# Kernel optimization log

Measured on AMD Instinct MI355X. Metric: run time of the kernel, lower is better.

Reference implementation:

```python
import jax, jax.numpy as jnp
import numpy as np

B, S, D, H = 2, 2048, 1024, 16
HD = D // H  # head dim = 64


def setup_inputs() -> dict:
    key = jax.random.key(0)
    ks = jax.random.split(key, 8)
    s = 0.02
    return {
        "Q": jax.random.normal(ks[0], (B, S, D), jnp.float32),
        "K": jax.random.normal(ks[1], (B, S, D), jnp.float32),
        "V": jax.random.normal(ks[2], (B, S, D), jnp.float32),
        "mask": jax.random.randint(ks[3], (1, 1, S, S), 0, 2, jnp.int32),
        "Wq": jax.random.normal(ks[4], (D, D), jnp.float32) * s,
        "bq": jnp.zeros((D,), jnp.float32),
        "Wk": jax.random.normal(ks[5], (D, D), jnp.float32) * s,
        "bk": jnp.zeros((D,), jnp.float32),
        "Wv": jax.random.normal(ks[6], (D, D), jnp.float32) * s,
        "bv": jnp.zeros((D,), jnp.float32),
        "Wo": jax.random.normal(ks[7], (D, D), jnp.float32) * s,
        "bo": jnp.zeros((D,), jnp.float32),
    }


def reference(Q, K, V, mask, Wq, bq, Wk, bk, Wv, bv, Wo, bo):
    b = Q.shape[0]
    # QKV projections, split into heads: [B,S,D] -> [B,H,S,HD]
    q = (Q @ Wq + bq).reshape(b, -1, H, HD).transpose(0, 2, 1, 3)
    k = (K @ Wk + bk).reshape(b, -1, H, HD).transpose(0, 2, 1, 3)
    v = (V @ Wv + bv).reshape(b, -1, H, HD).transpose(0, 2, 1, 3)
    # scaled dot-product attention with full [B,H,S,S] scores (as in source)
    scale = jnp.sqrt(jnp.asarray(HD, q.dtype))
    scores = jnp.einsum("bhqd,bhkd->bhqk", q, k) / scale
    scores = jnp.where(mask == 0, -jnp.inf, scores)
    attn = jax.nn.softmax(scores, axis=-1)
    ctx = jnp.einsum("bhqk,bhkd->bhqd", attn, v)
    # merge heads and output projection
    concat = ctx.transpose(0, 2, 1, 3).reshape(b, -1, H * HD)
    return concat @ Wo + bo
```

## Files before the change

kernel.cpp:

```cpp
#include <hip/hip_runtime.h>


using s8v = __attribute__((ext_vector_type(8))) short;
using f4v = __attribute__((ext_vector_type(4))) float;
typedef unsigned long long u64;

__device__ __forceinline__ unsigned short f2bf(float f) {
  union { float f; unsigned int u; } v; v.f = f;
  return (unsigned short)((v.u + 0x7fffu + ((v.u >> 16) & 1u)) >> 16);
}

__device__ __forceinline__ void gll16(const void* g, void* l) {
  __builtin_amdgcn_global_load_lds(
      (const __attribute__((address_space(1))) unsigned int*)g,
      (__attribute__((address_space(3))) unsigned int*)l, 16, 0, 0);
}

__global__ void prep_kernel(const float* __restrict__ Q, const float* __restrict__ K,
                            const float* __restrict__ V,
                            unsigned short* __restrict__ qb, unsigned short* __restrict__ kb,
                            unsigned short* __restrict__ vb,
                            const float* __restrict__ W0, const float* __restrict__ W1,
                            const float* __restrict__ W2, const float* __restrict__ W3,
                            unsigned short* __restrict__ T0, unsigned short* __restrict__ T1,
                            unsigned short* __restrict__ T2, unsigned short* __restrict__ T3,
                            const int* __restrict__ mask, u64* __restrict__ bm) {
  __shared__ unsigned short t[64][72];
  const int bid = blockIdx.x, tid = threadIdx.x;
  if (bid < 12288) {
    int z = bid >> 12;
    int idx = (bid & 4095) * 256 + tid;
    const float* in = (z == 0) ? Q : (z == 1) ? K : V;
    unsigned short* out = (z == 0) ? qb : (z == 1) ? kb : vb;
    float4 v = ((const float4*)in)[idx];
    ushort4 o;
    o.x = f2bf(v.x); o.y = f2bf(v.y); o.z = f2bf(v.z); o.w = f2bf(v.w);
    ((ushort4*)out)[idx] = o;
  } else if (bid < 13312) {
    int b = bid - 12288;
    int z = b >> 8, rem = b & 255;
    int k0 = (rem >> 4) * 64, n0 = (rem & 15) * 64;
    const float* W = (z == 0) ? W0 : (z == 1) ? W1 : (z == 2) ? W2 : W3;
    unsigned short* Wt = (z == 0) ? T0 : (z == 1) ? T1 : (z == 2) ? T2 : T3;
    for (int p = 0; p < 4; ++p) {
      int idx = p * 256 + tid;
      int row = idx >> 4, c4 = idx & 15;
      float4 v = *(const float4*)&W[(size_t)(k0 + row) * 1024 + n0 + c4 * 4];
      t[row][c4 * 4 + 0] = f2bf(v.x);
      t[row][c4 * 4 + 1] = f2bf(v.y);
      t[row][c4 * 4 + 2] = f2bf(v.z);
      t[row][c4 * 4 + 3] = f2bf(v.w);
    }
    __syncthreads();
    for (int p = 0; p < 2; ++p) {
      int idx = p * 256 + tid;
      int j = idx >> 3, c8 = idx & 7;
      unsigned short tmp[8];
      for (int i = 0; i < 8; ++i) tmp[i] = t[c8 * 8 + i][j];
      uint4 o;
      o.x = tmp[0] | ((unsigned)tmp[1] << 16);
      o.y = tmp[2] | ((unsigned)tmp[3] << 16);
      o.z = tmp[4] | ((unsigned)tmp[5] << 16);
      o.w = tmp[6] | ((unsigned)tmp[7] << 16);
      *(uint4*)&Wt[(size_t)(n0 + j) * 1024 + k0 + c8 * 8] = o;
    }
  } else {
    int b = bid - 13312;
    int gw = (b * 256 + tid) >> 6;
    int lane = tid & 63;
    int mv = mask[(size_t)gw * 64 + lane];
    u64 bal = __ballot(mv != 0);
    if (lane == 0) bm[gw] = bal;
  }
}

__global__ __launch_bounds__(256) void proj3_kernel(
    const unsigned short* __restrict__ A0, const unsigned short* __restrict__ A1,
    const unsigned short* __restrict__ A2,
    const unsigned short* __restrict__ W0, const unsigned short* __restrict__ W1,
    const unsigned short* __restrict__ W2,
    const float* __restrict__ b0, const float* __restrict__ b1, const float* __restrict__ b2,
    unsigned short* __restrict__ oq, unsigned short* __restrict__ ok,
    unsigned short* __restrict__ ovt) {
  const int z = blockIdx.z;
  const unsigned short* A  = (z == 0) ? A0 : (z == 1) ? A1 : A2;
  const unsigned short* Wt = (z == 0) ? W0 : (z == 1) ? W1 : W2;
  const float* bias        = (z == 0) ? b0 : (z == 1) ? b1 : b2;

  __shared__ __align__(16) unsigned short As[64 * 32];
  __shared__ __align__(16) unsigned short Bs[128 * 32];

  const int tid = threadIdx.x;
  const int lane = tid & 63, w = tid >> 6, ln = lane & 15, quad = lane >> 4;
  const int wm = (w & 1) * 32, wn = (w >> 1) * 64;
  const int m0 = blockIdx.x * 64, n0 = blockIdx.y * 128;

  const int slr = lane >> 2;
  const int schunk = (lane & 3) ^ ((lane >> 3) & 3);
  const int cfrag = (quad ^ ((ln >> 1) & 3)) * 8;

  f4v zero = {0.f, 0.f, 0.f, 0.f};
  f4v acc[2][4];
  for (int mi = 0; mi < 2; ++mi)
    for (int ni = 0; ni < 4; ++ni) acc[mi][ni] = zero;

  for (int kt = 0; kt < 1024; kt += 32) {
    __syncthreads();
    gll16(&A[(size_t)(m0 + w * 16 + slr) * 1024 + kt + schunk * 8],        &As[(w * 16) * 32]);
    gll16(&Wt[(size_t)(n0 + w * 32 + slr) * 1024 + kt + schunk * 8],       &Bs[(w * 32) * 32]);
    gll16(&Wt[(size_t)(n0 + w * 32 + 16 + slr) * 1024 + kt + schunk * 8],  &Bs[(w * 32 + 16) * 32]);
    __syncthreads();
    s8v a[2], b[4];
    for (int mi = 0; mi < 2; ++mi) a[mi] = *(const s8v*)&As[(wm + mi * 16 + ln) * 32 + cfrag];
    for (int ni = 0; ni < 4; ++ni) b[ni] = *(const s8v*)&Bs[(wn + ni * 16 + ln) * 32 + cfrag];
    if (z < 2) {
      for (int mi = 0; mi < 2; ++mi)
        for (int ni = 0; ni < 4; ++ni)
          acc[mi][ni] = __builtin_amdgcn_mfma_f32_16x16x32_bf16(a[mi], b[ni], acc[mi][ni], 0, 0, 0);
    } else {
      for (int mi = 0; mi < 2; ++mi)
        for (int ni = 0; ni < 4; ++ni)
          acc[mi][ni] = __builtin_amdgcn_mfma_f32_16x16x32_bf16(b[ni], a[mi], acc[mi][ni], 0, 0, 0);
    }
  }

  if (z < 2) {
    const float qscale = (z == 0) ? 0.18033688f : 1.0f;
    unsigned short* outp = (z == 0) ? oq : ok;
    for (int mi = 0; mi < 2; ++mi) {
      int rb = m0 + wm + mi * 16 + quad * 4;
      int b_ = rb >> 11;
      for (int ni = 0; ni < 4; ++ni) {
        int col = n0 + wn + ni * 16 + ln;
        float bvv = bias[col];
        int h = col >> 6, hd = col & 63;
        size_t ob = (size_t)(b_ * 16 + h) * 2048;
        for (int r = 0; r < 4; ++r) {
          int s = (rb + r) & 2047;
          outp[(ob + s) * 64 + hd] = f2bf((acc[mi][ni][r] + bvv) * qscale);
        }
      }
    }
  } else {
    for (int ni = 0; ni < 4; ++ni) {
      for (int r = 0; r < 4; ++r) {
        int colw = n0 + wn + ni * 16 + quad * 4 + r;
        int h = colw >> 6, hd = colw & 63;
        float bvv = bias[colw];
        for (int mi = 0; mi < 2; ++mi) {
          int sg = m0 + wm + mi * 16 + ln;
          int b_ = sg >> 11, ss = sg & 2047;
          ovt[((size_t)(b_ * 16 + h) * 64 + hd) * 2048 + ss] = f2bf(acc[mi][ni][r] + bvv);
        }
      }
    }
  }
}

__global__ __launch_bounds__(256) void flash_kernel(
    const unsigned short* __restrict__ q, const unsigned short* __restrict__ k,
    const unsigned short* __restrict__ vt, const u64* __restrict__ bm,
    unsigned short* __restrict__ ctx) {
  __shared__ __align__(16) unsigned short qp_s[128][72];
  __shared__ __align__(16) unsigned short k_s[64][72];
  __shared__ __align__(16) unsigned short v_s[80][72];

  const int tid = threadIdx.x;
  const int lane = tid & 63, w = tid >> 6, ln = lane & 15, quad = lane >> 4;
  const int q0 = blockIdx.x * 128;
  const int bh = blockIdx.y;
  const unsigned short* qg  = q  + ((size_t)bh * 2048 + q0) * 64;
  const unsigned short* kgb = k  + (size_t)bh * 2048 * 64;
  const unsigned short* vgb = vt + (size_t)bh * 64 * 2048;

  for (int j = 0; j < 5; ++j) {
    int idx = j * 256 + tid;
    if (idx < 16 * 72) ((unsigned short*)v_s[64])[idx] = 0;
  }
  for (int p = 0; p < 4; ++p) {
    int c = p * 256 + tid;
    int row = c >> 3, c8 = c & 7;
    *(uint4*)&qp_s[row][c8 * 8] = *(const uint4*)&qg[(size_t)row * 64 + c8 * 8];
  }
  __syncthreads();
  if (tid < 64) v_s[64][tid] = 0x3F80;
  __syncthreads();

  s8v aq[2][2];
  for (int s = 0; s < 2; ++s)
    for (int h = 0; h < 2; ++h)
      aq[s][h] = *(const s8v*)&qp_s[s * 64 + w * 16 + ln][h * 32 + quad * 8];
  s8v bones0 = *(const s8v*)&v_s[64 + ln][quad * 8];
  s8v bones1 = *(const s8v*)&v_s[64 + ln][32 + quad * 8];

  const int srow0 = tid >> 3, sc8 = tid & 7;
  const int srow1 = 32 + srow0;

  const u64* bmr0 = bm + (size_t)(q0 + w * 16 + ln) * 32;
  const u64* bmr1 = bmr0 + 64 * 32;

  uint4 kr0 = *(const uint4*)&kgb[(size_t)srow0 * 64 + sc8 * 8];
  uint4 kr1 = *(const uint4*)&kgb[(size_t)srow1 * 64 + sc8 * 8];
  uint4 vr0 = *(const uint4*)&vgb[(size_t)srow0 * 2048 + sc8 * 8];
  uint4 vr1 = *(const uint4*)&vgb[(size_t)srow1 * 2048 + sc8 * 8];
  u64 mwc[2], mwn[2];
  mwc[0] = bmr0[0];
  mwc[1] = bmr1[0];

  f4v zero = {0.f, 0.f, 0.f, 0.f};
  f4v l_acc[2];
  f4v o_acc[2][4];
  for (int s = 0; s < 2; ++s) {
    l_acc[s] = zero;
    for (int ni = 0; ni < 4; ++ni) o_acc[s][ni] = zero;
  }

  for (int kt = 0; kt < 2048; kt += 64) {
    *(uint4*)&k_s[srow0][sc8 * 8] = kr0;
    *(uint4*)&k_s[srow1][sc8 * 8] = kr1;
    *(uint4*)&v_s[srow0][sc8 * 8] = vr0;
    *(uint4*)&v_s[srow1][sc8 * 8] = vr1;
    if (kt + 64 < 2048) {
      int ktn = kt + 64;
      kr0 = *(const uint4*)&kgb[(size_t)(ktn + srow0) * 64 + sc8 * 8];
      kr1 = *(const uint4*)&kgb[(size_t)(ktn + srow1) * 64 + sc8 * 8];
      vr0 = *(const uint4*)&vgb[(size_t)srow0 * 2048 + ktn + sc8 * 8];
      vr1 = *(const uint4*)&vgb[(size_t)srow1 * 2048 + ktn + sc8 * 8];
      int ktcn = ktn >> 6;
      mwn[0] = bmr0[ktcn];
      mwn[1] = bmr1[ktcn];
    }
    __syncthreads();

    f4v sc[2][4];
    for (int ni = 0; ni < 4; ++ni) {
      s8v ak0 = *(const s8v*)&k_s[ni * 16 + ln][quad * 8];
      s8v ak1 = *(const s8v*)&k_s[ni * 16 + ln][32 + quad * 8];
      for (int s = 0; s < 2; ++s) {
        f4v t = zero;
        t = __builtin_amdgcn_mfma_f32_16x16x32_bf16(ak0, aq[s][0], t, 0, 0, 0);
        t = __builtin_amdgcn_mfma_f32_16x16x32_bf16(ak1, aq[s][1], t, 0, 0, 0);
        sc[s][ni] = t;
      }
    }

    for (int s = 0; s < 2; ++s) {
      u64 m = mwc[s] >> (quad * 4);
      unsigned mlo = (unsigned)m, mhi = (unsigned)(m >> 32);
      for (int ni = 0; ni < 4; ++ni) {
        unsigned msel = ((ni < 2) ? mlo : mhi) >> ((ni & 1) * 16);
        unsigned u0 = __float_as_uint(__builtin_amdgcn_exp2f(sc[s][ni][0]) * (float)(msel & 1u));
        unsigned u1 = __float_as_uint(__builtin_amdgcn_exp2f(sc[s][ni][1]) * (float)((msel >> 1) & 1u));
        unsigned u2 = __float_as_uint(__builtin_amdgcn_exp2f(sc[s][ni][2]) * (float)((msel >> 2) & 1u));
        unsigned u3 = __float_as_uint(__builtin_amdgcn_exp2f(sc[s][ni][3]) * (float)((msel >> 3) & 1u));
        unsigned plo = __builtin_amdgcn_perm(u1, u0, 0x07060302);
        unsigned phi = __builtin_amdgcn_perm(u3, u2, 0x07060302);
        *(u64*)&qp_s[s * 64 + w * 16 + ln][ni * 16 + quad * 4] = plo | ((u64)phi << 32);
      }
      mwc[s] = mwn[s];
    }

    s8v ap[2][2];
    for (int s = 0; s < 2; ++s)
      for (int h = 0; h < 2; ++h)
        ap[s][h] = *(const s8v*)&qp_s[s * 64 + w * 16 + ln][h * 32 + quad * 8];
    for (int ni = 0; ni < 4; ++ni) {
      s8v bv0 = *(const s8v*)&v_s[ni * 16 + ln][quad * 8];
      s8v bv1 = *(const s8v*)&v_s[ni * 16 + ln][32 + quad * 8];
      for (int s = 0; s < 2; ++s) {
        o_acc[s][ni] = __builtin_amdgcn_mfma_f32_16x16x32_bf16(ap[s][0], bv0, o_acc[s][ni], 0, 0, 0);
        o_acc[s][ni] = __builtin_amdgcn_mfma_f32_16x16x32_bf16(ap[s][1], bv1, o_acc[s][ni], 0, 0, 0);
      }
    }
    for (int s = 0; s < 2; ++s) {
      l_acc[s] = __builtin_amdgcn_mfma_f32_16x16x32_bf16(ap[s][0], bones0, l_acc[s], 0, 0, 0);
      l_acc[s] = __builtin_amdgcn_mfma_f32_16x16x32_bf16(ap[s][1], bones1, l_acc[s], 0, 0, 0);
    }
    __syncthreads();
  }

  int b_ = bh >> 4, h = bh & 15;
  for (int s = 0; s < 2; ++s) {
    for (int r = 0; r < 4; ++r) {
      float lr = __shfl(l_acc[s][r], quad * 16);
      float inv = 1.f / lr;
      int srow = q0 + s * 64 + w * 16 + quad * 4 + r;
      size_t base = ((size_t)b_ * 2048 + srow) * 1024 + h * 64;
      for (int ni = 0; ni < 4; ++ni)
        ctx[base + ni * 16 + ln] = f2bf(o_acc[s][ni][r] * inv);
    }
  }
}

__global__ __launch_bounds__(256) void gemm_out_kernel(
    const unsigned short* __restrict__ A, const unsigned short* __restrict__ Wt,
    const float* __restrict__ bias, float* __restrict__ out) {
  __shared__ __align__(16) unsigned short As[64 * 32];
  __shared__ __align__(16) unsigned short Bs[128 * 32];

  const int tid = threadIdx.x;
  const int lane = tid & 63, w = tid >> 6, ln = lane & 15, quad = lane >> 4;
  const int wm = (w & 1) * 32, wn = (w >> 1) * 64;
  const int m0 = blockIdx.x * 64, n0 = blockIdx.y * 128;

  const int slr = lane >> 2;
  const int schunk = (lane & 3) ^ ((lane >> 3) & 3);
  const int cfrag = (quad ^ ((ln >> 1) & 3)) * 8;

  f4v zero = {0.f, 0.f, 0.f, 0.f};
  f4v acc[2][4];
  for (int mi = 0; mi < 2; ++mi)
    for (int ni = 0; ni < 4; ++ni) acc[mi][ni] = zero;

  for (int kt = 0; kt < 1024; kt += 32) {
    __syncthreads();
    gll16(&A[(size_t)(m0 + w * 16 + slr) * 1024 + kt + schunk * 8],        &As[(w * 16) * 32]);
    gll16(&Wt[(size_t)(n0 + w * 32 + slr) * 1024 + kt + schunk * 8],       &Bs[(w * 32) * 32]);
    gll16(&Wt[(size_t)(n0 + w * 32 + 16 + slr) * 1024 + kt + schunk * 8],  &Bs[(w * 32 + 16) * 32]);
    __syncthreads();
    s8v a[2], b[4];
    for (int mi = 0; mi < 2; ++mi) a[mi] = *(const s8v*)&As[(wm + mi * 16 + ln) * 32 + cfrag];
    for (int ni = 0; ni < 4; ++ni) b[ni] = *(const s8v*)&Bs[(wn + ni * 16 + ln) * 32 + cfrag];
    for (int mi = 0; mi < 2; ++mi)
      for (int ni = 0; ni < 4; ++ni)
        acc[mi][ni] = __builtin_amdgcn_mfma_f32_16x16x32_bf16(a[mi], b[ni], acc[mi][ni], 0, 0, 0);
  }

  for (int mi = 0; mi < 2; ++mi) {
    int rb = m0 + wm + mi * 16 + quad * 4;
    for (int ni = 0; ni < 4; ++ni) {
      int col = n0 + wn + ni * 16 + ln;
      float bvv = bias[col];
      for (int r = 0; r < 4; ++r)
        out[(size_t)(rb + r) * 1024 + col] = acc[mi][ni][r] + bvv;
    }
  }
}

extern "C" void kernel_launch(void* const* d_in, const int* in_sizes, int n_in,
                              void* d_out, int out_size, void* d_ws, size_t ws_size,
                              hipStream_t stream) {
  const float* Q  = (const float*)d_in[0];
  const float* K  = (const float*)d_in[1];
  const float* V  = (const float*)d_in[2];
  const int* mask = (const int*)d_in[3];
  const float* Wq = (const float*)d_in[4];
  const float* bq = (const float*)d_in[5];
  const float* Wk = (const float*)d_in[6];
  const float* bk = (const float*)d_in[7];
  const float* Wv = (const float*)d_in[8];
  const float* bv = (const float*)d_in[9];
  const float* Wo = (const float*)d_in[10];
  const float* bo = (const float*)d_in[11];
  float* out = (float*)d_out;

  char* ws = (char*)d_ws;
  const size_t MB = 1u << 20;
  unsigned short* qb  = (unsigned short*)(ws + 0 * MB);
  unsigned short* kb  = (unsigned short*)(ws + 8 * MB);
  unsigned short* vb  = (unsigned short*)(ws + 16 * MB);
  unsigned short* wqt = (unsigned short*)(ws + 24 * MB);
  unsigned short* wkt = (unsigned short*)(ws + 26 * MB);
  unsigned short* wvt = (unsigned short*)(ws + 28 * MB);
  unsigned short* wot = (unsigned short*)(ws + 30 * MB);
  unsigned short* qh  = (unsigned short*)(ws + 32 * MB);
  unsigned short* kh  = (unsigned short*)(ws + 40 * MB);
  unsigned short* vth = (unsigned short*)(ws + 48 * MB);
  u64* bm             = (u64*)(ws + 56 * MB);
  unsigned short* ctx = (unsigned short*)(ws + 16 * MB);

  prep_kernel<<<29696, 256, 0, stream>>>(Q, K, V, qb, kb, vb,
                                         Wq, Wk, Wv, Wo, wqt, wkt, wvt, wot,
                                         mask, bm);
  proj3_kernel<<<dim3(64, 8, 3), 256, 0, stream>>>(qb, kb, vb, wqt, wkt, wvt,
                                                   bq, bk, bv, qh, kh, vth);
  flash_kernel<<<dim3(16, 32), 256, 0, stream>>>(qh, kh, vth, bm, ctx);
  gemm_out_kernel<<<dim3(64, 8), 256, 0, stream>>>(ctx, wot, bo, out);
}
```

Before: 260.8 us.

## Split attention over key halves with atomic accumulation and add combine kernel

The flash kernel now splits the key dimension into two chunks, doubling the grid to 1024 blocks. Each block atomically adds its unnormalized output and row-sum into fp32 global buffers. A new combine kernel normalizes these and writes the bf16 context. This is valid without a running max only because the code never subtracts one, so partial sums add directly. It also swaps grid x/y ordering in the projection and output GEMMs so blocks sharing the same M-tile run adjacently. The aim is better CU occupancy on the attention stage, at the cost of two memsets, atomic traffic and an extra kernel launch.

```diff
diff --git a/kernel.cpp b/kernel.cpp
--- a/kernel.cpp
+++ b/kernel.cpp
@@ -93,7 +93,7 @@
   const int tid = threadIdx.x;
   const int lane = tid & 63, w = tid >> 6, ln = lane & 15, quad = lane >> 4;
   const int wm = (w & 1) * 32, wn = (w >> 1) * 64;
-  const int m0 = blockIdx.x * 64, n0 = blockIdx.y * 128;
+  const int n0 = blockIdx.x * 128, m0 = blockIdx.y * 64;
 
   const int slr = lane >> 2;
   const int schunk = (lane & 3) ^ ((lane >> 3) & 3);
@@ -160,18 +160,19 @@
 __global__ __launch_bounds__(256) void flash_kernel(
     const unsigned short* __restrict__ q, const unsigned short* __restrict__ k,
     const unsigned short* __restrict__ vt, const u64* __restrict__ bm,
-    unsigned short* __restrict__ ctx) {
+    float* __restrict__ o_glob, float* __restrict__ l_glob) {
   __shared__ __align__(16) unsigned short qp_s[128][72];
   __shared__ __align__(16) unsigned short k_s[64][72];
   __shared__ __align__(16) unsigned short v_s[80][72];
 
   const int tid = threadIdx.x;
   const int lane = tid & 63, w = tid >> 6, ln = lane & 15, quad = lane >> 4;
-  const int q0 = blockIdx.x * 128;
+  const int qt = blockIdx.x & 15, kc = blockIdx.x >> 4;
+  const int q0 = qt * 128;
   const int bh = blockIdx.y;
   const unsigned short* qg  = q  + ((size_t)bh * 2048 + q0) * 64;
-  const unsigned short* kgb = k  + (size_t)bh * 2048 * 64;
-  const unsigned short* vgb = vt + (size_t)bh * 64 * 2048;
+  const unsigned short* kgb = k  + ((size_t)bh * 2048 + kc * 1024) * 64;
+  const unsigned short* vgb = vt + (size_t)bh * 64 * 2048 + kc * 1024;
 
   for (int j = 0; j < 5; ++j) {
     int idx = j * 256 + tid;
@@ -196,7 +197,7 @@
   const int srow0 = tid >> 3, sc8 = tid & 7;
   const int srow1 = 32 + srow0;
 
-  const u64* bmr0 = bm + (size_t)(q0 + w * 16 + ln) * 32;
+  const u64* bmr0 = bm + (size_t)(q0 + w * 16 + ln) * 32 + kc * 16;
   const u64* bmr1 = bmr0 + 64 * 32;
 
   uint4 kr0 = *(const uint4*)&kgb[(size_t)srow0 * 64 + sc8 * 8];
@@ -215,12 +216,12 @@
     for (int ni = 0; ni < 4; ++ni) o_acc[s][ni] = zero;
   }
 
-  for (int kt = 0; kt < 2048; kt += 64) {
+  for (int kt = 0; kt < 1024; kt += 64) {
     *(uint4*)&k_s[srow0][sc8 * 8] = kr0;
     *(uint4*)&k_s[srow1][sc8 * 8] = kr1;
     *(uint4*)&v_s[srow0][sc8 * 8] = vr0;
     *(uint4*)&v_s[srow1][sc8 * 8] = vr1;
-    if (kt + 64 < 2048) {
+    if (kt + 64 < 1024) {
       int ktn = kt + 64;
       kr0 = *(const uint4*)&kgb[(size_t)(ktn + srow0) * 64 + sc8 * 8];
       kr1 = *(const uint4*)&kgb[(size_t)(ktn + srow1) * 64 + sc8 * 8];
@@ -279,17 +280,38 @@
     __syncthreads();
   }
 
+  float* og = o_glob + (size_t)bh * 2048 * 64;
+  for (int s = 0; s < 2; ++s) {
+    for (int ni = 0; ni < 4; ++ni)
+      for (int r = 0; r < 4; ++r) {
+        int srow = q0 + s * 64 + w * 16 + quad * 4 + r;
+        atomicAdd(&og[(size_t)srow * 64 + ni * 16 + ln], o_acc[s][ni][r]);
+      }
+    if (ln == 0) {
+      for (int r = 0; r < 4; ++r) {
+        int srow = q0 + s * 64 + w * 16 + quad * 4 + r;
+        atomicAdd(&l_glob[bh * 2048 + srow], l_acc[s][r]);
+      }
+    }
+  }
+}
+
+__global__ void combine_kernel(const float* __restrict__ o, const float* __restrict__ l,
+                               unsigned short* __restrict__ ctx) {
+  int idx = blockIdx.x * 256 + threadIdx.x;
+  float4 v = ((const float4*)o)[idx];
+  int e = idx * 4;
+  int row = e >> 6;
+  float inv = 1.f / l[row];
+  int bh = row >> 11, srow = row & 2047;
   int b_ = bh >> 4, h = bh & 15;
-  for (int s = 0; s < 2; ++s) {
-    for (int r = 0; r < 4; ++r) {
-      float lr = __shfl(l_acc[s][r], quad * 16);
-      float inv = 1.f / lr;
-      int srow = q0 + s * 64 + w * 16 + quad * 4 + r;
-      size_t base = ((size_t)b_ * 2048 + srow) * 1024 + h * 64;
-      for (int ni = 0; ni < 4; ++ni)
-        ctx[base + ni * 16 + ln] = f2bf(o_acc[s][ni][r] * inv);
-    }
-  }
+  int hd = e & 63;
+  ushort4 pk;
+  pk.x = f2bf(v.x * inv);
+  pk.y = f2bf(v.y * inv);
+  pk.z = f2bf(v.z * inv);
+  pk.w = f2bf(v.w * inv);
+  *(ushort4*)&ctx[((size_t)(b_ * 2048 + srow)) * 1024 + h * 64 + hd] = pk;
 }
 
 __global__ __launch_bounds__(256) void gemm_out_kernel(
@@ -301,7 +323,7 @@
   const int tid = threadIdx.x;
   const int lane = tid & 63, w = tid >> 6, ln = lane & 15, quad = lane >> 4;
   const int wm = (w & 1) * 32, wn = (w >> 1) * 64;
-  const int m0 = blockIdx.x * 64, n0 = blockIdx.y * 128;
+  const int n0 = blockIdx.x * 128, m0 = blockIdx.y * 64;
 
   const int slr = lane >> 2;
   const int schunk = (lane & 3) ^ ((lane >> 3) & 3);
@@ -367,13 +389,18 @@
   unsigned short* kh  = (unsigned short*)(ws + 40 * MB);
   unsigned short* vth = (unsigned short*)(ws + 48 * MB);
   u64* bm             = (u64*)(ws + 56 * MB);
+  float* l_glob       = (float*)(ws + 56 * MB + 786432);
+  float* o_glob       = (float*)(ws + 0 * MB);
   unsigned short* ctx = (unsigned short*)(ws + 16 * MB);
 
   prep_kernel<<<29696, 256, 0, stream>>>(Q, K, V, qb, kb, vb,
                                          Wq, Wk, Wv, Wo, wqt, wkt, wvt, wot,
                                          mask, bm);
-  proj3_kernel<<<dim3(64, 8, 3), 256, 0, stream>>>(qb, kb, vb, wqt, wkt, wvt,
+  proj3_kernel<<<dim3(8, 64, 3), 256, 0, stream>>>(qb, kb, vb, wqt, wkt, wvt,
                                                    bq, bk, bv, qh, kh, vth);
-  flash_kernel<<<dim3(16, 32), 256, 0, stream>>>(qh, kh, vth, bm, ctx);
-  gemm_out_kernel<<<dim3(64, 8), 256, 0, stream>>>(ctx, wot, bo, out);
-}
+  hipMemsetAsync(o_glob, 0, 16 * MB, stream);
+  hipMemsetAsync(l_glob, 0, 262144, stream);
+  flash_kernel<<<dim3(32, 32), 256, 0, stream>>>(qh, kh, vth, bm, o_glob, l_glob);
+  combine_kernel<<<4096, 256, 0, stream>>>(o_glob, l_glob, ctx);
+  gemm_out_kernel<<<dim3(8, 64), 256, 0, stream>>>(ctx, wot, bo, out);
+}
```

After: 289.2 us. 1.11x slower.
